# Optimization experiments

Hardware: AMD Instinct MI355X
Metric: run time of the kernel (lower is better)

Reference implementation:

```python
import jax, jax.numpy as jnp
import numpy as np
from jax import lax

B, NK, NQ, DK, DV, H = 4, 4096, 4096, 64, 64, 256


def _linear_params(key, fan_in, fan_out):
    kw, kb = jax.random.split(key)
    lim = 1.0 / np.sqrt(fan_in)
    w = jax.random.uniform(kw, (fan_out, fan_in), jnp.float32, -lim, lim)
    b = jax.random.uniform(kb, (fan_out,), jnp.float32, -lim, lim)
    return w, b


def setup_inputs() -> dict:
    key = jax.random.key(0)
    ks = jax.random.split(key, 9)
    inp = {
        "KEY": jax.random.normal(ks[0], (B, NK, DK), jnp.float32),
        "VALUE": jax.random.normal(ks[1], (B, NK, DV), jnp.float32),
        "QUERY": jax.random.normal(ks[2], (B, NQ, DK), jnp.float32),
    }
    inp["W1_w"], inp["W1_b"] = _linear_params(ks[3], DK, H)
    inp["W2_w"], inp["W2_b"] = _linear_params(ks[4], H, H)
    inp["W3_w"], inp["W3_b"] = _linear_params(ks[5], H, DK)
    inp["Wo1_w"], inp["Wo1_b"] = _linear_params(ks[6], DK, H)
    inp["Wo2_w"], inp["Wo2_b"] = _linear_params(ks[7], H, H)
    inp["Wo3_w"], inp["Wo3_b"] = _linear_params(ks[8], H, DV)
    return inp


def _mlp(x, w1, b1, w2, b2, w3, b3):
    h = jax.nn.relu(jnp.einsum('bnd,hd->bnh', x, w1) + b1)
    h = jax.nn.relu(jnp.einsum('bnh,gh->bng', h, w2) + b2)
    return jnp.einsum('bng,og->bno', h, w3) + b3


def _l1_cdist(K, Q):
    # K: [b,nk,d], Q: [b,nq,d] -> [b,nk,nq]; scan over feature dim to avoid
    # materializing the [b,nk,nq,d] difference tensor.
    b, nk, _ = K.shape
    nq = Q.shape[1]

    def body(acc, kq):
        k, q = kq  # [b,nk], [b,nq]
        return acc + jnp.abs(k[:, :, None] - q[:, None, :]), None

    init = jnp.zeros((b, nk, nq), K.dtype)
    score, _ = lax.scan(body, init, (jnp.moveaxis(K, -1, 0), jnp.moveaxis(Q, -1, 0)))
    return score


def reference(KEY, VALUE, QUERY, W1_w, W1_b, W2_w, W2_b, W3_w, W3_b,
              Wo1_w, Wo1_b, Wo2_w, Wo2_b, Wo3_w, Wo3_b):
    Wk = _mlp(KEY, W1_w, W1_b, W2_w, W2_b, W3_w, W3_b)
    Wq = _mlp(QUERY, W1_w, W1_b, W2_w, W2_b, W3_w, W3_b)
    Wo = _mlp(QUERY, Wo1_w, Wo1_b, Wo2_w, Wo2_b, Wo3_w, Wo3_b)
    KEY_scale = KEY * Wk          # [b,nk,dk]
    QUERY_scale = QUERY * Wq      # [b,nq,dk]
    score = _l1_cdist(KEY_scale, QUERY_scale)            # [b,nk,nq]
    attn = jax.nn.softmax(-(score * score) * 0.5, axis=1)  # softmax over keys
    context = jnp.einsum('bik,bij->bkj', attn, VALUE)    # [b,nq,dv]
    # dropout is identity in eval mode
    return context * Wo
```

## Files before the change

### kernel.cpp

```cpp
#include <hip/hip_runtime.h>
#include <hip/hip_bf16.h>
#include <stdint.h>

#define B_DIM 4
#define NKK 4096
#define NQQ 4096
#define DD 64
#define HH 256

typedef __attribute__((ext_vector_type(4))) float floatx4;
typedef __attribute__((ext_vector_type(2))) float floatx2;
typedef __attribute__((ext_vector_type(8))) short bf16x8;

__device__ __forceinline__ float fexp2(float x) { return __builtin_amdgcn_exp2f(x); }
__device__ __forceinline__ unsigned fbits(float x) { return __float_as_uint(x); }
__device__ __forceinline__ float bf2f(unsigned short u) { return __uint_as_float(((unsigned)u) << 16); }

__device__ __forceinline__ floatx2 pk_sub(floatx2 a, floatx2 b) {
  floatx2 d;
  asm("v_pk_add_f32 %0, %1, %2 neg_lo:[0,1] neg_hi:[0,1]" : "=v"(d) : "v"(a), "v"(b));
  return d;
}

__device__ __forceinline__ void splitbf(float x, unsigned short& h, unsigned short& l) {
  unsigned u = fbits(x);
  unsigned hu = (u + 0x7fff + ((u >> 16) & 1)) & 0xffff0000u;
  h = (unsigned short)(hu >> 16);
  l = (unsigned short)(fbits(x - __uint_as_float(hu)) >> 16);
}

#define FSTRIDE 68
#define FSTRIDE4 17
#define PSTRIDE 36

__global__ __launch_bounds__(256) void wsplit_kernel(
    const float* __restrict__ W1a, const float* __restrict__ W2a, const float* __restrict__ W3a,
    const float* __restrict__ W1b, const float* __restrict__ W2b, const float* __restrict__ W3b,
    unsigned short* __restrict__ sp)
{
  int idx = blockIdx.x * 256 + threadIdx.x;
  const int set = idx >= 98304;
  int r = idx - set * 98304;
  unsigned short* base = sp + (size_t)set * 196608;
  const float* src;
  unsigned short *dh, *dl;
  int j;
  if (r < 16384)      { src = set ? W1b : W1a; dh = base;          dl = base + 16384;  j = r; }
  else if (r < 81920) { src = set ? W2b : W2a; dh = base + 32768;  dl = base + 98304;  j = r - 16384; }
  else                { src = set ? W3b : W3a; dh = base + 163840; dl = base + 180224; j = r - 81920; }
  unsigned short h, l;
  splitbf(src[j], h, l);
  dh[j] = h; dl[j] = l;
}

__global__ __launch_bounds__(256) void vtrans_kernel(
    const float* __restrict__ V, unsigned short* __restrict__ Vt)
{
  __shared__ unsigned short t[64][80];
  const int tid = threadIdx.x;
  const int b = blockIdx.y;
  const int k0 = blockIdx.x * 64;
  const float4* V4 = (const float4*)V;
  {
    const int r = tid & 63;
    const int c4 = tid >> 6;
#pragma unroll
    for (int j = 0; j < 4; ++j) {
      float4 f = V4[((size_t)(b * NKK + k0 + r)) * 16 + c4 * 4 + j];
      const int d0 = c4 * 16 + j * 4;
      t[d0 + 0][r] = (unsigned short)(fbits(f.x) >> 16);
      t[d0 + 1][r] = (unsigned short)(fbits(f.y) >> 16);
      t[d0 + 2][r] = (unsigned short)(fbits(f.z) >> 16);
      t[d0 + 3][r] = (unsigned short)(fbits(f.w) >> 16);
    }
  }
  __syncthreads();
  {
    const int d = tid >> 2;
    const int kc = tid & 3;
    uint4 u0 = *(const uint4*)&t[d][kc * 16];
    uint4 u1 = *(const uint4*)&t[d][kc * 16 + 8];
    unsigned short* dst = Vt + ((size_t)(b * 64 + d)) * NKK + k0 + kc * 16;
    *(uint4*)dst = u0;
    *(uint4*)(dst + 8) = u1;
  }
}

#define HSTRIDE 264
__global__ __launch_bounds__(512, 1) void mlpmm_kernel(
    const float* __restrict__ KEY, const float* __restrict__ QUERY,
    const float* __restrict__ B1a, const float* __restrict__ B2a, const float* __restrict__ B3a,
    const float* __restrict__ B1b, const float* __restrict__ B2b, const float* __restrict__ B3b,
    const unsigned short* __restrict__ sp,
    float* __restrict__ Ks, float* __restrict__ Qs, float* __restrict__ Wo)
{
  __shared__ unsigned short Xh[64][72], Xl[64][72];
  __shared__ unsigned short Hsh[64][HSTRIDE], Hsl[64][HSTRIDE];
  const int tid = threadIdx.x;
  const int w = tid >> 6;
  const int lane = tid & 63;
  const int l15 = lane & 15;
  const int quad = lane >> 4;

  const int g = blockIdx.x;
  const float* X;
  float* outp;
  int mulx, t0;
  const unsigned short* wb;
  const float *b1, *b2, *b3;
  if (g < 256)      { X = KEY;   outp = Ks; mulx = 1; t0 = g * 64;         wb = sp;          b1 = B1a; b2 = B2a; b3 = B3a; }
  else if (g < 512) { X = QUERY; outp = Qs; mulx = 1; t0 = (g - 256) * 64; wb = sp;          b1 = B1a; b2 = B2a; b3 = B3a; }
  else              { X = QUERY; outp = Wo; mulx = 0; t0 = (g - 512) * 64; wb = sp + 196608; b1 = B1b; b2 = B2b; b3 = B3b; }
  const unsigned short* W1h = wb;
  const unsigned short* W1l = wb + 16384;
  const unsigned short* W2h = wb + 32768;
  const unsigned short* W2l = wb + 98304;
  const unsigned short* W3h = wb + 163840;
  const unsigned short* W3l = wb + 180224;

  {
    const int t = tid >> 3;
    const int c = (tid & 7) * 8;
    float4 a = *(const float4*)&X[(size_t)(t0 + t) * 64 + c];
    float4 b = *(const float4*)&X[(size_t)(t0 + t) * 64 + c + 4];
    float v[8] = {a.x, a.y, a.z, a.w, b.x, b.y, b.z, b.w};
    unsigned short hs[8], ls[8];
#pragma unroll
    for (int e = 0; e < 8; ++e) splitbf(v[e], hs[e], ls[e]);
    uint4 uh = make_uint4(hs[0] | ((unsigned)hs[1] << 16), hs[2] | ((unsigned)hs[3] << 16),
                          hs[4] | ((unsigned)hs[5] << 16), hs[6] | ((unsigned)hs[7] << 16));
    uint4 ul = make_uint4(ls[0] | ((unsigned)ls[1] << 16), ls[2] | ((unsigned)ls[3] << 16),
                          ls[4] | ((unsigned)ls[5] << 16), ls[6] | ((unsigned)ls[7] << 16));
    *(uint4*)&Xh[t][c] = uh;
    *(uint4*)&Xl[t][c] = ul;
  }
  __syncthreads();

  {
    floatx4 acc[4][2];
#pragma unroll
    for (int nb = 0; nb < 2; ++nb) {
      const float bias = b1[(w * 2 + nb) * 16 + l15];
#pragma unroll
      for (int mb = 0; mb < 4; ++mb) acc[mb][nb] = (floatx4){bias, bias, bias, bias};
    }
#pragma unroll
    for (int kb = 0; kb < 2; ++kb) {
      bf16x8 Ah[4], Al[4];
#pragma unroll
      for (int mb = 0; mb < 4; ++mb) {
        Ah[mb] = *(const bf16x8*)&Xh[mb * 16 + l15][kb * 32 + quad * 8];
        Al[mb] = *(const bf16x8*)&Xl[mb * 16 + l15][kb * 32 + quad * 8];
      }
#pragma unroll
      for (int nb = 0; nb < 2; ++nb) {
        const int n0 = (w * 2 + nb) * 16;
        bf16x8 Bh = *(const bf16x8*)&W1h[(size_t)(n0 + l15) * 64 + kb * 32 + quad * 8];
        bf16x8 Bl = *(const bf16x8*)&W1l[(size_t)(n0 + l15) * 64 + kb * 32 + quad * 8];
#pragma unroll
        for (int mb = 0; mb < 4; ++mb) {
          acc[mb][nb] = __builtin_amdgcn_mfma_f32_16x16x32_bf16(Ah[mb], Bh, acc[mb][nb], 0, 0, 0);
          acc[mb][nb] = __builtin_amdgcn_mfma_f32_16x16x32_bf16(Al[mb], Bh, acc[mb][nb], 0, 0, 0);
          acc[mb][nb] = __builtin_amdgcn_mfma_f32_16x16x32_bf16(Ah[mb], Bl, acc[mb][nb], 0, 0, 0);
        }
      }
    }
#pragma unroll
    for (int mb = 0; mb < 4; ++mb)
#pragma unroll
      for (int nb = 0; nb < 2; ++nb) {
        const int col = (w * 2 + nb) * 16 + l15;
#pragma unroll
        for (int r = 0; r < 4; ++r) {
          const int row = mb * 16 + quad * 4 + r;
          float v = fmaxf(acc[mb][nb][r], 0.0f);
          unsigned short h, l;
          splitbf(v, h, l);
          Hsh[row][col] = h;
          Hsl[row][col] = l;
        }
      }
  }
  __syncthreads();

  {
    floatx4 acc2[4][2];
#pragma unroll
    for (int nb = 0; nb < 2; ++nb) {
      const float bias = b2[(w * 2 + nb) * 16 + l15];
#pragma unroll
      for (int mb = 0; mb < 4; ++mb) acc2[mb][nb] = (floatx4){bias, bias, bias, bias};
    }
#pragma unroll
    for (int kb = 0; kb < 8; ++kb) {
      bf16x8 Ah[4], Al[4];
#pragma unroll
      for (int mb = 0; mb < 4; ++mb) {
        Ah[mb] = *(const bf16x8*)&Hsh[mb * 16 + l15][kb * 32 + quad * 8];
        Al[mb] = *(const bf16x8*)&Hsl[mb * 16 + l15][kb * 32 + quad * 8];
      }
#pragma unroll
      for (int nb = 0; nb < 2; ++nb) {
        const int n0 = (w * 2 + nb) * 16;
        bf16x8 Bh = *(const bf16x8*)&W2h[(size_t)(n0 + l15) * 256 + kb * 32 + quad * 8];
        bf16x8 Bl = *(const bf16x8*)&W2l[(size_t)(n0 + l15) * 256 + kb * 32 + quad * 8];
#pragma unroll
        for (int mb = 0; mb < 4; ++mb) {
          acc2[mb][nb] = __builtin_amdgcn_mfma_f32_16x16x32_bf16(Ah[mb], Bh, acc2[mb][nb], 0, 0, 0);
          acc2[mb][nb] = __builtin_amdgcn_mfma_f32_16x16x32_bf16(Al[mb], Bh, acc2[mb][nb], 0, 0, 0);
          acc2[mb][nb] = __builtin_amdgcn_mfma_f32_16x16x32_bf16(Ah[mb], Bl, acc2[mb][nb], 0, 0, 0);
        }
      }
    }
    __syncthreads();
#pragma unroll
    for (int mb = 0; mb < 4; ++mb)
#pragma unroll
      for (int nb = 0; nb < 2; ++nb) {
        const int col = (w * 2 + nb) * 16 + l15;
#pragma unroll
        for (int r = 0; r < 4; ++r) {
          const int row = mb * 16 + quad * 4 + r;
          float v = fmaxf(acc2[mb][nb][r], 0.0f);
          unsigned short h, l;
          splitbf(v, h, l);
          Hsh[row][col] = h;
          Hsl[row][col] = l;
        }
      }
  }
  __syncthreads();

  {
    const int mp = (w >> 2) * 2;
    const int n0 = (w & 3) * 16;
    const float bias = b3[n0 + l15];
    floatx4 acc3[2];
#pragma unroll
    for (int m = 0; m < 2; ++m) acc3[m] = (floatx4){bias, bias, bias, bias};
#pragma unroll
    for (int kb = 0; kb < 8; ++kb) {
      bf16x8 Ah[2], Al[2];
#pragma unroll
      for (int m = 0; m < 2; ++m) {
        Ah[m] = *(const bf16x8*)&Hsh[(mp + m) * 16 + l15][kb * 32 + quad * 8];
        Al[m] = *(const bf16x8*)&Hsl[(mp + m) * 16 + l15][kb * 32 + quad * 8];
      }
      bf16x8 Bh = *(const bf16x8*)&W3h[(size_t)(n0 + l15) * 256 + kb * 32 + quad * 8];
      bf16x8 Bl = *(const bf16x8*)&W3l[(size_t)(n0 + l15) * 256 + kb * 32 + quad * 8];
#pragma unroll
      for (int m = 0; m < 2; ++m) {
        acc3[m] = __builtin_amdgcn_mfma_f32_16x16x32_bf16(Ah[m], Bh, acc3[m], 0, 0, 0);
        acc3[m] = __builtin_amdgcn_mfma_f32_16x16x32_bf16(Al[m], Bh, acc3[m], 0, 0, 0);
        acc3[m] = __builtin_amdgcn_mfma_f32_16x16x32_bf16(Ah[m], Bl, acc3[m], 0, 0, 0);
      }
    }
#pragma unroll
    for (int m = 0; m < 2; ++m)
#pragma unroll
      for (int r = 0; r < 4; ++r) {
        const int row = (mp + m) * 16 + quad * 4 + r;
        const int col = n0 + l15;
        float v = acc3[m][r];
        if (mulx) v *= (bf2f(Xh[row][col]) + bf2f(Xl[row][col]));
        outp[(size_t)(t0 + row) * 64 + col] = v;
      }
  }
}

template <bool PARTIAL>
__global__ __launch_bounds__(256, 3) void attn_kernel(
    const float* __restrict__ Ksg, const float* __restrict__ Qsg,
    const unsigned short* __restrict__ Vtg, const float* __restrict__ Wog,
    float* __restrict__ outp,
    float* __restrict__ Pm, float* __restrict__ Pl, float* __restrict__ PO)
{
  __shared__ float qsA[32 * FSTRIDE];
  __shared__ float ksA[4][32 * FSTRIDE];
  __shared__ unsigned short psB[4][32 * PSTRIDE];
  __shared__ float abA[4][32];

  const int tid  = threadIdx.x;
  const int w    = tid >> 6;
  const int lane = tid & 63;
  const int lq   = lane >> 3;
  const int lk   = lane & 7;
  const int l15  = lane & 15;
  const int quad = lane >> 4;
  const int b    = blockIdx.y;
  const int qt   = blockIdx.x * 32;

  {
    const int row = tid >> 3;
    const int c0  = (tid & 7) * 2;
    const float4* Q4 = (const float4*)Qsg;
    float4 g0 = Q4[(size_t)(b * NQQ + qt + row) * 16 + c0];
    float4 g1 = Q4[(size_t)(b * NQQ + qt + row) * 16 + c0 + 1];
    *(float4*)&qsA[row * FSTRIDE + c0 * 4]     = g0;
    *(float4*)&qsA[row * FSTRIDE + c0 * 4 + 4] = g1;
  }
  __syncthreads();

  float m_i[4], l_i[4];
  floatx4 acc[2][4];
#pragma unroll
  for (int i = 0; i < 4; ++i) { m_i[i] = -3.0e38f; l_i[i] = 0.0f; }
#pragma unroll
  for (int mb = 0; mb < 2; ++mb)
#pragma unroll
    for (int nb = 0; nb < 4; ++nb)
#pragma unroll
      for (int r = 0; r < 4; ++r) acc[mb][nb][r] = 0.0f;

  int kstart, iters;
  if (PARTIAL) {
    const int slice = blockIdx.z * 4 + w;
    iters  = (slice < 8) ? 11 : 10;
    kstart = (slice < 8) ? slice * 352 : 2816 + (slice - 8) * 320;
  } else {
    iters  = 32;
    kstart = w * 1024;
  }
  const float4* K4 = (const float4*)Ksg;
  const float NEG_HALF_LOG2E = -0.72134752044448170f;

  const int krow = (lane >> 4);
  const int kci  = lane & 15;

  const unsigned short* vg0 = Vtg + ((size_t)b * 64 + l15) * NKK + kstart + quad * 8;

  float4 kpre[8];
  uint4 vtpre[4];
#pragma unroll
  for (int c = 0; c < 8; ++c)
    kpre[c] = K4[(size_t)(b * NKK + kstart + c * 4 + krow) * 16 + kci];
#pragma unroll
  for (int nb = 0; nb < 4; ++nb)
    vtpre[nb] = *(const uint4*)(vg0 + (size_t)nb * 16 * NKK);

  const floatx4* qb = (const floatx4*)&qsA[lq * FSTRIDE];
  const floatx4* kb = (const floatx4*)&ksA[w][lk * FSTRIDE];

  for (int it = 0; it < iters; ++it) {
#pragma unroll
    for (int c = 0; c < 8; ++c)
      *(float4*)&ksA[w][(c * 4 + krow) * FSTRIDE + kci * 4] = kpre[c];

    {
      const int itn = (it + 1 < iters) ? it + 1 : it;
#pragma unroll
      for (int c = 0; c < 8; ++c)
        kpre[c] = K4[(size_t)(b * NKK + kstart + itn * 32 + c * 4 + krow) * 16 + kci];
    }

    float s[4][4];
#pragma unroll
    for (int i = 0; i < 4; ++i)
#pragma unroll
      for (int j = 0; j < 4; ++j) s[i][j] = 0.0f;

#pragma unroll
    for (int dc = 0; dc < 16; ++dc) {
      floatx4 qv[4], kv[4];
#pragma unroll
      for (int i = 0; i < 4; ++i) qv[i] = qb[i * (8 * FSTRIDE4) + dc];
#pragma unroll
      for (int j = 0; j < 4; ++j) kv[j] = kb[j * (8 * FSTRIDE4) + dc];
#pragma unroll
      for (int i = 0; i < 4; ++i) {
        const floatx2 qlo = qv[i].lo, qhi = qv[i].hi;
#pragma unroll
        for (int j = 0; j < 4; ++j) {
          floatx2 d0 = pk_sub(qlo, kv[j].lo);
          floatx2 d1 = pk_sub(qhi, kv[j].hi);
          s[i][j] += __builtin_fabsf(d0.x);
          s[i][j] += __builtin_fabsf(d0.y);
          s[i][j] += __builtin_fabsf(d1.x);
          s[i][j] += __builtin_fabsf(d1.y);
        }
      }
    }

    float a_row[4];
#pragma unroll
    for (int i = 0; i < 4; ++i) {
      float smin = fminf(fminf(s[i][0], s[i][1]), fminf(s[i][2], s[i][3]));
      smin = fminf(smin, __shfl_xor(smin, 1));
      smin = fminf(smin, __shfl_xor(smin, 2));
      smin = fminf(smin, __shfl_xor(smin, 4));
      const float tmax = smin * smin * NEG_HALF_LOG2E;
      const float mn = fmaxf(m_i[i], tmax);
      a_row[i] = fexp2(m_i[i] - mn);
      m_i[i] = mn;
      float ps = 0.0f;
#pragma unroll
      for (int j = 0; j < 4; ++j) {
        const float sv = s[i][j];
        const float e = fexp2(fmaf(sv * NEG_HALF_LOG2E, sv, -mn));
        ps += e;
        psB[w][(lq + 8 * i) * PSTRIDE + lk + 8 * j] = (unsigned short)(fbits(e) >> 16);
      }
      l_i[i] = fmaf(l_i[i], a_row[i], ps);
    }
    if (lk == 0) {
#pragma unroll
      for (int i = 0; i < 4; ++i) abA[w][lq + 8 * i] = a_row[i];
    }

    {
      bf16x8 afrag[2];
#pragma unroll
      for (int mb = 0; mb < 2; ++mb)
        afrag[mb] = *(const bf16x8*)&psB[w][(mb * 16 + l15) * PSTRIDE + quad * 8];

      const floatx4 arv0 = *(const floatx4*)&abA[w][quad * 4];
      const floatx4 arv1 = *(const floatx4*)&abA[w][16 + quad * 4];

#pragma unroll
      for (int nb = 0; nb < 4; ++nb) {
        bf16x8 bfrag = __builtin_bit_cast(bf16x8, vtpre[nb]);
        acc[0][nb] *= arv0;
        acc[1][nb] *= arv1;
        acc[0][nb] = __builtin_amdgcn_mfma_f32_16x16x32_bf16(afrag[0], bfrag, acc[0][nb], 0, 0, 0);
        acc[1][nb] = __builtin_amdgcn_mfma_f32_16x16x32_bf16(afrag[1], bfrag, acc[1][nb], 0, 0, 0);
      }
    }

    {
      const int itn = (it + 1 < iters) ? it + 1 : it;
#pragma unroll
      for (int nb = 0; nb < 4; ++nb)
        vtpre[nb] = *(const uint4*)(vg0 + (size_t)nb * 16 * NKK + itn * 32);
    }
  }

#pragma unroll
  for (int i = 0; i < 4; ++i) {
    float l = l_i[i];
    l += __shfl_xor(l, 1);
    l += __shfl_xor(l, 2);
    l += __shfl_xor(l, 4);
    l_i[i] = l;
  }
  float* ovl = (float*)&psB[w][0];
  if (lk == 0) {
#pragma unroll
    for (int i = 0; i < 4; ++i) {
      ovl[lq + 8 * i]      = m_i[i];
      ovl[32 + lq + 8 * i] = l_i[i];
    }
  }
#pragma unroll
  for (int mb = 0; mb < 2; ++mb)
#pragma unroll
    for (int nb = 0; nb < 4; ++nb)
#pragma unroll
      for (int r = 0; r < 4; ++r)
        ksA[w][(mb * 16 + quad * 4 + r) * 64 + nb * 16 + l15] = acc[mb][nb][r];
  __syncthreads();

  {
    const int q = tid >> 3;
    const int dbase = (tid & 7) * 8;
    const float m0 = ((const float*)&psB[0][0])[q];
    const float m1 = ((const float*)&psB[1][0])[q];
    const float m2 = ((const float*)&psB[2][0])[q];
    const float m3 = ((const float*)&psB[3][0])[q];
    const float M = fmaxf(fmaxf(m0, m1), fmaxf(m2, m3));
    const float s0 = fexp2(m0 - M), s1 = fexp2(m1 - M);
    const float s2v = fexp2(m2 - M), s3 = fexp2(m3 - M);
    const float L = ((const float*)&psB[0][0])[32 + q] * s0 +
                    ((const float*)&psB[1][0])[32 + q] * s1 +
                    ((const float*)&psB[2][0])[32 + q] * s2v +
                    ((const float*)&psB[3][0])[32 + q] * s3;
    if (PARTIAL) {
      const size_t p = (size_t)(blockIdx.z * 4 + b) * 128 + blockIdx.x;
      if (dbase == 0) { Pm[p * 32 + q] = M; Pl[p * 32 + q] = L; }
      float* dst = PO + p * 2048 + q * 64 + dbase;
#pragma unroll
      for (int c = 0; c < 8; ++c) {
        const int d = dbase + c;
        dst[c] = s0 * ksA[0][q * 64 + d] + s1 * ksA[1][q * 64 + d] +
                 s2v * ksA[2][q * 64 + d] + s3 * ksA[3][q * 64 + d];
      }
    } else {
      const float rL = 1.0f / L;
      const size_t gbase = (size_t)(b * NQQ + qt + q) * 64 + dbase;
#pragma unroll
      for (int c = 0; c < 8; ++c) {
        const int d = dbase + c;
        float o = s0 * ksA[0][q * 64 + d] + s1 * ksA[1][q * 64 + d] +
                  s2v * ksA[2][q * 64 + d] + s3 * ksA[3][q * 64 + d];
        outp[gbase + c] = o * rL * Wog[gbase + c];
      }
    }
  }
}

__global__ __launch_bounds__(256) void amerge_kernel(
    const float* __restrict__ Pm, const float* __restrict__ Pl,
    const float* __restrict__ PO, const float* __restrict__ Wog,
    float* __restrict__ outp)
{
  const int tid = threadIdx.x;
  const int qt = blockIdx.x;
  const int b = blockIdx.y;
  const int q = tid >> 3;
  const int dbase = (tid & 7) * 8;
  size_t p[3];
  float mv[3], lv[3];
#pragma unroll
  for (int s = 0; s < 3; ++s) {
    p[s] = (size_t)(s * 4 + b) * 128 + qt;
    mv[s] = Pm[p[s] * 32 + q];
    lv[s] = Pl[p[s] * 32 + q];
  }
  const float M = fmaxf(fmaxf(mv[0], mv[1]), mv[2]);
  float wsum = 0.0f, wgt[3];
#pragma unroll
  for (int s = 0; s < 3; ++s) { wgt[s] = fexp2(mv[s] - M); wsum += wgt[s] * lv[s]; }
  const float rL = 1.0f / wsum;
  const size_t g = ((size_t)b * NQQ + qt * 32 + q) * 64 + dbase;
#pragma unroll
  for (int c = 0; c < 8; ++c) {
    float o = 0.0f;
#pragma unroll
    for (int s = 0; s < 3; ++s) o += wgt[s] * PO[p[s] * 2048 + q * 64 + dbase + c];
    outp[g + c] = o * rL * Wog[g + c];
  }
}

extern "C" void kernel_launch(void* const* d_in, const int* in_sizes, int n_in,
                              void* d_out, int out_size, void* d_ws, size_t ws_size,
                              hipStream_t stream) {
  (void)in_sizes; (void)n_in; (void)out_size;
  const float* KEY   = (const float*)d_in[0];
  const float* VALUE = (const float*)d_in[1];
  const float* QUERY = (const float*)d_in[2];
  const float* W1w = (const float*)d_in[3];
  const float* W1b = (const float*)d_in[4];
  const float* W2w = (const float*)d_in[5];
  const float* W2b = (const float*)d_in[6];
  const float* W3w = (const float*)d_in[7];
  const float* W3b = (const float*)d_in[8];
  const float* Wo1w = (const float*)d_in[9];
  const float* Wo1b = (const float*)d_in[10];
  const float* Wo2w = (const float*)d_in[11];
  const float* Wo2b = (const float*)d_in[12];
  const float* Wo3w = (const float*)d_in[13];
  const float* Wo3b = (const float*)d_in[14];

  float* ws = (float*)d_ws;
  const size_t tsz = (size_t)B_DIM * NKK * DD;
  float* Ks = ws;
  float* Qs = ws + tsz;
  float* Wo = ws + 2 * tsz;
  unsigned short* Vtg = (unsigned short*)(ws + 3 * tsz);
  unsigned short* sp  = Vtg + tsz;
  float* Pm = ws + 3 * tsz + tsz / 2 + 196608;
  float* Pl = Pm + 49152;
  float* PO = Pl + 49152;
  float* outf = (float*)d_out;

  const size_t ws_need = (size_t)(3 * tsz + tsz / 2 + 196608 + 2 * 49152 + 3145728) * 4;
  const bool partial = ws_size >= ws_need;

  wsplit_kernel<<<dim3(768), 256, 0, stream>>>(W1w, W2w, W3w, Wo1w, Wo2w, Wo3w, sp);
  vtrans_kernel<<<dim3(NKK / 64, B_DIM), 256, 0, stream>>>(VALUE, Vtg);
  mlpmm_kernel<<<dim3(768), 512, 0, stream>>>(
      KEY, QUERY, W1b, W2b, W3b, Wo1b, Wo2b, Wo3b, sp, Ks, Qs, Wo);
  if (partial) {
    attn_kernel<true><<<dim3(NQQ / 32, B_DIM, 3), 256, 0, stream>>>(
        Ks, Qs, Vtg, Wo, outf, Pm, Pl, PO);
    amerge_kernel<<<dim3(NQQ / 32, B_DIM), 256, 0, stream>>>(Pm, Pl, PO, Wo, outf);
  } else {
    attn_kernel<false><<<dim3(NQQ / 32, B_DIM, 1), 256, 0, stream>>>(
        Ks, Qs, Vtg, Wo, outf, Pm, Pl, PO);
  }
}
```

Measured before the change: 412.7 us.

## Swizzle LDS tiles, alias buffers, raise occupancy, and use power-of-two key splits

Replaces the padded shared-memory tiles for Q and K with XOR-swizzled unpadded layouts. The P and alpha buffers are aliased into the per-wave K region, shrinking LDS to 40KB so launch bounds can ask for 4 blocks per CU. The key dimension is now split into 4 (or 2) even slices instead of 3 uneven ones, with a templated merge kernel. The trade-off is more partial-output traffic and a larger merge, plus an extra barrier before the epilogue.

```diff
diff --git a/kernel.cpp b/kernel.cpp
--- a/kernel.cpp
+++ b/kernel.cpp
@@ -29,8 +29,6 @@
   l = (unsigned short)(fbits(x - __uint_as_float(hu)) >> 16);
 }
 
-#define FSTRIDE 68
-#define FSTRIDE4 17
 #define PSTRIDE 36
 
 __global__ __launch_bounds__(256) void wsplit_kernel(
@@ -268,17 +266,15 @@
   }
 }
 
-template <bool PARTIAL>
-__global__ __launch_bounds__(256, 3) void attn_kernel(
+template <int Z>
+__global__ __launch_bounds__(256, 4) void attn_kernel(
     const float* __restrict__ Ksg, const float* __restrict__ Qsg,
     const unsigned short* __restrict__ Vtg, const float* __restrict__ Wog,
     float* __restrict__ outp,
     float* __restrict__ Pm, float* __restrict__ Pl, float* __restrict__ PO)
 {
-  __shared__ float qsA[32 * FSTRIDE];
-  __shared__ float ksA[4][32 * FSTRIDE];
-  __shared__ unsigned short psB[4][32 * PSTRIDE];
-  __shared__ float abA[4][32];
+  __shared__ float lds[10240];
+  float* qsA = lds;
 
   const int tid  = threadIdx.x;
   const int w    = tid >> 6;
@@ -290,14 +286,17 @@
   const int b    = blockIdx.y;
   const int qt   = blockIdx.x * 32;
 
+  float* ksw = lds + 2048 + w * 2048;
+
   {
     const int row = tid >> 3;
     const int c0  = (tid & 7) * 2;
     const float4* Q4 = (const float4*)Qsg;
     float4 g0 = Q4[(size_t)(b * NQQ + qt + row) * 16 + c0];
     float4 g1 = Q4[(size_t)(b * NQQ + qt + row) * 16 + c0 + 1];
-    *(float4*)&qsA[row * FSTRIDE + c0 * 4]     = g0;
-    *(float4*)&qsA[row * FSTRIDE + c0 * 4 + 4] = g1;
+    const int r7 = row & 7;
+    *(float4*)&qsA[row * 64 + ((c0 ^ r7) << 2)]       = g0;
+    *(float4*)&qsA[row * 64 + (((c0 + 1) ^ r7) << 2)] = g1;
   }
   __syncthreads();
 
@@ -313,10 +312,10 @@
       for (int r = 0; r < 4; ++r) acc[mb][nb][r] = 0.0f;
 
   int kstart, iters;
-  if (PARTIAL) {
+  if (Z > 1) {
     const int slice = blockIdx.z * 4 + w;
-    iters  = (slice < 8) ? 11 : 10;
-    kstart = (slice < 8) ? slice * 352 : 2816 + (slice - 8) * 320;
+    iters  = (NKK / (4 * Z)) / 32;
+    kstart = slice * (NKK / (4 * Z));
   } else {
     iters  = 32;
     kstart = w * 1024;
@@ -338,13 +337,19 @@
   for (int nb = 0; nb < 4; ++nb)
     vtpre[nb] = *(const uint4*)(vg0 + (size_t)nb * 16 * NKK);
 
-  const floatx4* qb = (const floatx4*)&qsA[lq * FSTRIDE];
-  const floatx4* kb = (const floatx4*)&ksA[w][lk * FSTRIDE];
+  const char* qbase = (const char*)qsA + (lq << 8);
+  const char* kbase = (const char*)ksw + (lk << 8);
+  const int lq16 = lq << 4, lk16 = lk << 4;
+  unsigned short* psw = (unsigned short*)ksw;
+  float* abw = (float*)((char*)ksw + 2304);
 
   for (int it = 0; it < iters; ++it) {
 #pragma unroll
-    for (int c = 0; c < 8; ++c)
-      *(float4*)&ksA[w][(c * 4 + krow) * FSTRIDE + kci * 4] = kpre[c];
+    for (int c = 0; c < 8; ++c) {
+      const int row  = c * 4 + krow;
+      const int slot = kci ^ (row & 7);
+      *(float4*)((char*)ksw + row * 256 + (slot << 4)) = kpre[c];
+    }
 
     {
       const int itn = (it + 1 < iters) ? it + 1 : it;
@@ -361,11 +366,13 @@
 
 #pragma unroll
     for (int dc = 0; dc < 16; ++dc) {
+      const floatx4* qp = (const floatx4*)(qbase + (((dc << 4) ^ lq16)));
+      const floatx4* kp = (const floatx4*)(kbase + (((dc << 4) ^ lk16)));
       floatx4 qv[4], kv[4];
 #pragma unroll
-      for (int i = 0; i < 4; ++i) qv[i] = qb[i * (8 * FSTRIDE4) + dc];
-#pragma unroll
-      for (int j = 0; j < 4; ++j) kv[j] = kb[j * (8 * FSTRIDE4) + dc];
+      for (int i = 0; i < 4; ++i) qv[i] = qp[i * 128];
+#pragma unroll
+      for (int j = 0; j < 4; ++j) kv[j] = kp[j * 128];
 #pragma unroll
       for (int i = 0; i < 4; ++i) {
         const floatx2 qlo = qv[i].lo, qhi = qv[i].hi;
@@ -398,23 +405,23 @@
         const float sv = s[i][j];
         const float e = fexp2(fmaf(sv * NEG_HALF_LOG2E, sv, -mn));
         ps += e;
-        psB[w][(lq + 8 * i) * PSTRIDE + lk + 8 * j] = (unsigned short)(fbits(e) >> 16);
+        psw[(lq + 8 * i) * PSTRIDE + lk + 8 * j] = (unsigned short)(fbits(e) >> 16);
       }
       l_i[i] = fmaf(l_i[i], a_row[i], ps);
     }
     if (lk == 0) {
 #pragma unroll
-      for (int i = 0; i < 4; ++i) abA[w][lq + 8 * i] = a_row[i];
+      for (int i = 0; i < 4; ++i) abw[lq + 8 * i] = a_row[i];
     }
 
     {
       bf16x8 afrag[2];
 #pragma unroll
       for (int mb = 0; mb < 2; ++mb)
-        afrag[mb] = *(const bf16x8*)&psB[w][(mb * 16 + l15) * PSTRIDE + quad * 8];
-
-      const floatx4 arv0 = *(const floatx4*)&abA[w][quad * 4];
-      const floatx4 arv1 = *(const floatx4*)&abA[w][16 + quad * 4];
+        afrag[mb] = *(const bf16x8*)&psw[(mb * 16 + l15) * PSTRIDE + quad * 8];
+
+      const floatx4 arv0 = *(const floatx4*)&abw[quad * 4];
+      const floatx4 arv1 = *(const floatx4*)&abw[16 + quad * 4];
 
 #pragma unroll
       for (int nb = 0; nb < 4; ++nb) {
@@ -442,12 +449,15 @@
     l += __shfl_xor(l, 4);
     l_i[i] = l;
   }
-  float* ovl = (float*)&psB[w][0];
-  if (lk == 0) {
-#pragma unroll
-    for (int i = 0; i < 4; ++i) {
-      ovl[lq + 8 * i]      = m_i[i];
-      ovl[32 + lq + 8 * i] = l_i[i];
+  __syncthreads();
+  {
+    float* ovl = qsA + w * 64;
+    if (lk == 0) {
+#pragma unroll
+      for (int i = 0; i < 4; ++i) {
+        ovl[lq + 8 * i]      = m_i[i];
+        ovl[32 + lq + 8 * i] = l_i[i];
+      }
     }
   }
 #pragma unroll
@@ -456,47 +466,44 @@
     for (int nb = 0; nb < 4; ++nb)
 #pragma unroll
       for (int r = 0; r < 4; ++r)
-        ksA[w][(mb * 16 + quad * 4 + r) * 64 + nb * 16 + l15] = acc[mb][nb][r];
+        ksw[(mb * 16 + quad * 4 + r) * 64 + nb * 16 + l15] = acc[mb][nb][r];
   __syncthreads();
 
   {
     const int q = tid >> 3;
     const int dbase = (tid & 7) * 8;
-    const float m0 = ((const float*)&psB[0][0])[q];
-    const float m1 = ((const float*)&psB[1][0])[q];
-    const float m2 = ((const float*)&psB[2][0])[q];
-    const float m3 = ((const float*)&psB[3][0])[q];
+    const float m0 = qsA[q],       l0 = qsA[32 + q];
+    const float m1 = qsA[64 + q],  l1 = qsA[96 + q];
+    const float m2 = qsA[128 + q], l2 = qsA[160 + q];
+    const float m3 = qsA[192 + q], l3 = qsA[224 + q];
     const float M = fmaxf(fmaxf(m0, m1), fmaxf(m2, m3));
     const float s0 = fexp2(m0 - M), s1 = fexp2(m1 - M);
     const float s2v = fexp2(m2 - M), s3 = fexp2(m3 - M);
-    const float L = ((const float*)&psB[0][0])[32 + q] * s0 +
-                    ((const float*)&psB[1][0])[32 + q] * s1 +
-                    ((const float*)&psB[2][0])[32 + q] * s2v +
-                    ((const float*)&psB[3][0])[32 + q] * s3;
-    if (PARTIAL) {
+    const float L = l0 * s0 + l1 * s1 + l2 * s2v + l3 * s3;
+    const float* ob = lds + 2048 + q * 64 + dbase;
+    if (Z > 1) {
       const size_t p = (size_t)(blockIdx.z * 4 + b) * 128 + blockIdx.x;
       if (dbase == 0) { Pm[p * 32 + q] = M; Pl[p * 32 + q] = L; }
       float* dst = PO + p * 2048 + q * 64 + dbase;
 #pragma unroll
       for (int c = 0; c < 8; ++c) {
-        const int d = dbase + c;
-        dst[c] = s0 * ksA[0][q * 64 + d] + s1 * ksA[1][q * 64 + d] +
-                 s2v * ksA[2][q * 64 + d] + s3 * ksA[3][q * 64 + d];
+        dst[c] = s0 * ob[c] + s1 * ob[2048 + c] +
+                 s2v * ob[4096 + c] + s3 * ob[6144 + c];
       }
     } else {
       const float rL = 1.0f / L;
       const size_t gbase = (size_t)(b * NQQ + qt + q) * 64 + dbase;
 #pragma unroll
       for (int c = 0; c < 8; ++c) {
-        const int d = dbase + c;
-        float o = s0 * ksA[0][q * 64 + d] + s1 * ksA[1][q * 64 + d] +
-                  s2v * ksA[2][q * 64 + d] + s3 * ksA[3][q * 64 + d];
+        float o = s0 * ob[c] + s1 * ob[2048 + c] +
+                  s2v * ob[4096 + c] + s3 * ob[6144 + c];
         outp[gbase + c] = o * rL * Wog[gbase + c];
       }
     }
   }
 }
 
+template <int NS>
 __global__ __launch_bounds__(256) void amerge_kernel(
     const float* __restrict__ Pm, const float* __restrict__ Pl,
     const float* __restrict__ PO, const float* __restrict__ Wog,
@@ -507,25 +514,27 @@
   const int b = blockIdx.y;
   const int q = tid >> 3;
   const int dbase = (tid & 7) * 8;
-  size_t p[3];
-  float mv[3], lv[3];
-#pragma unroll
-  for (int s = 0; s < 3; ++s) {
+  size_t p[NS];
+  float mv[NS], lv[NS];
+#pragma unroll
+  for (int s = 0; s < NS; ++s) {
     p[s] = (size_t)(s * 4 + b) * 128 + qt;
     mv[s] = Pm[p[s] * 32 + q];
     lv[s] = Pl[p[s] * 32 + q];
   }
-  const float M = fmaxf(fmaxf(mv[0], mv[1]), mv[2]);
-  float wsum = 0.0f, wgt[3];
-#pragma unroll
-  for (int s = 0; s < 3; ++s) { wgt[s] = fexp2(mv[s] - M); wsum += wgt[s] * lv[s]; }
+  float M = mv[0];
+#pragma unroll
+  for (int s = 1; s < NS; ++s) M = fmaxf(M, mv[s]);
+  float wsum = 0.0f, wgt[NS];
+#pragma unroll
+  for (int s = 0; s < NS; ++s) { wgt[s] = fexp2(mv[s] - M); wsum += wgt[s] * lv[s]; }
   const float rL = 1.0f / wsum;
   const size_t g = ((size_t)b * NQQ + qt * 32 + q) * 64 + dbase;
 #pragma unroll
   for (int c = 0; c < 8; ++c) {
     float o = 0.0f;
 #pragma unroll
-    for (int s = 0; s < 3; ++s) o += wgt[s] * PO[p[s] * 2048 + q * 64 + dbase + c];
+    for (int s = 0; s < NS; ++s) o += wgt[s] * PO[p[s] * 2048 + q * 64 + dbase + c];
     outp[g + c] = o * rL * Wog[g + c];
   }
 }
@@ -558,23 +567,28 @@
   unsigned short* Vtg = (unsigned short*)(ws + 3 * tsz);
   unsigned short* sp  = Vtg + tsz;
   float* Pm = ws + 3 * tsz + tsz / 2 + 196608;
-  float* Pl = Pm + 49152;
-  float* PO = Pl + 49152;
+  float* Pl = Pm + 65536;
+  float* PO = Pl + 65536;
   float* outf = (float*)d_out;
 
-  const size_t ws_need = (size_t)(3 * tsz + tsz / 2 + 196608 + 2 * 49152 + 3145728) * 4;
-  const bool partial = ws_size >= ws_need;
+  const size_t fbase = 3 * tsz + tsz / 2 + 196608 + 2 * 65536;
+  const size_t need4 = (fbase + (size_t)16 * 128 * 2048) * 4;
+  const size_t need2 = (fbase + (size_t)8 * 128 * 2048) * 4;
 
   wsplit_kernel<<<dim3(768), 256, 0, stream>>>(W1w, W2w, W3w, Wo1w, Wo2w, Wo3w, sp);
   vtrans_kernel<<<dim3(NKK / 64, B_DIM), 256, 0, stream>>>(VALUE, Vtg);
   mlpmm_kernel<<<dim3(768), 512, 0, stream>>>(
       KEY, QUERY, W1b, W2b, W3b, Wo1b, Wo2b, Wo3b, sp, Ks, Qs, Wo);
-  if (partial) {
-    attn_kernel<true><<<dim3(NQQ / 32, B_DIM, 3), 256, 0, stream>>>(
+  if (ws_size >= need4) {
+    attn_kernel<4><<<dim3(NQQ / 32, B_DIM, 4), 256, 0, stream>>>(
         Ks, Qs, Vtg, Wo, outf, Pm, Pl, PO);
-    amerge_kernel<<<dim3(NQQ / 32, B_DIM), 256, 0, stream>>>(Pm, Pl, PO, Wo, outf);
+    amerge_kernel<4><<<dim3(NQQ / 32, B_DIM), 256, 0, stream>>>(Pm, Pl, PO, Wo, outf);
+  } else if (ws_size >= need2) {
+    attn_kernel<2><<<dim3(NQQ / 32, B_DIM, 2), 256, 0, stream>>>(
+        Ks, Qs, Vtg, Wo, outf, Pm, Pl, PO);
+    amerge_kernel<2><<<dim3(NQQ / 32, B_DIM), 256, 0, stream>>>(Pm, Pl, PO, Wo, outf);
   } else {
-    attn_kernel<false><<<dim3(NQQ / 32, B_DIM, 1), 256, 0, stream>>>(
+    attn_kernel<1><<<dim3(NQQ / 32, B_DIM, 1), 256, 0, stream>>>(
         Ks, Qs, Vtg, Wo, outf, Pm, Pl, PO);
   }
 }
```

New measurement: 556.2 us. 34.8% more time.
